# Performance work log

Hardware: AMD Instinct MI355X
Metric: run time of the kernel (lower is better)

The kernel has to match this reference:

```python
import jax, jax.numpy as jnp
import numpy as np

K = 4          # temporal_depth
IN_SIZE = 1024 # conv input channels
DN = ('NCDHW', 'OIDHW', 'NCDHW')


def setup_inputs() -> dict:
    key = jax.random.key(0)
    ks = jax.random.split(key, 12)
    B, T, C, H, W = 1, 8, IN_SIZE, 14, 14
    s = 0.02
    return {
        'videos': jax.random.normal(ks[0], (B, T, C, H, W), dtype=jnp.float32),
        # Conv3d(in_size, in_size, 3, padding='same')
        'conv1_w': jax.random.normal(ks[1], (IN_SIZE, IN_SIZE, 3, 3, 3), dtype=jnp.float32) * s,
        'conv1_b': jax.random.normal(ks[2], (IN_SIZE,), dtype=jnp.float32) * s,
        # Conv3d(in_size, 512, 3, padding='same')
        'conv2_w': jax.random.normal(ks[3], (512, IN_SIZE, 3, 3, 3), dtype=jnp.float32) * s,
        'conv2_b': jax.random.normal(ks[4], (512,), dtype=jnp.float32) * s,
        # Linear(512,512) -> Linear(512,512) -> Linear(512,128), torch (out,in) layout
        'l1_w': jax.random.normal(ks[5], (512, 512), dtype=jnp.float32) * s,
        'l1_b': jax.random.normal(ks[6], (512,), dtype=jnp.float32) * s,
        'l2_w': jax.random.normal(ks[7], (512, 512), dtype=jnp.float32) * s,
        'l2_b': jax.random.normal(ks[8], (512,), dtype=jnp.float32) * s,
        'l3_w': jax.random.normal(ks[9], (128, 512), dtype=jnp.float32) * s,
        'l3_b': jax.random.normal(ks[10], (128,), dtype=jnp.float32) * s,
    }


def reference(videos, conv1_w, conv1_b, conv2_w, conv2_b,
              l1_w, l1_b, l2_w, l2_b, l3_w, l3_b):
    B, T, C, H, W = videos.shape
    # prepend k zero frames, as in the torch code
    padded = jnp.concatenate(
        [jnp.zeros((B, K, C, H, W), videos.dtype), videos], axis=1)
    # window o covers padded frames [o, o+K) -> strictly-past original frames
    idx = jnp.arange(T)[:, None] + jnp.arange(K)[None, :]      # (T, K)
    win = padded[:, idx]                                        # (B, T, K, C, H, W)
    # permute(1,0,2,3): channels first, depth=K -> batch all windows together
    win = win.transpose(0, 1, 3, 2, 4, 5).reshape(B * T, C, K, H, W)
    # Conv3d + ReLU + Conv3d + ReLU, each with 'same' zero padding per window
    h = jax.lax.conv_general_dilated(win, conv1_w, (1, 1, 1), 'SAME',
                                     dimension_numbers=DN)
    h = jax.nn.relu(h + conv1_b[None, :, None, None, None])
    h = jax.lax.conv_general_dilated(h, conv2_w, (1, 1, 1), 'SAME',
                                     dimension_numbers=DN)
    h = jax.nn.relu(h + conv2_b[None, :, None, None, None])
    # MaxPool3d over the full (D,H,W) extent == global max per channel
    pooled = jnp.max(h, axis=(2, 3, 4))                         # (B*T, 512)
    x = jax.nn.relu(pooled @ l1_w.T + l1_b)
    x = jax.nn.relu(x @ l2_w.T + l2_b)
    x = jax.nn.relu(x @ l3_w.T + l3_b)                          # (B*T, 128)
    return x.reshape(B, T, 128)
```

## Files before the change

### kernel.cpp

```cpp
#include <hip/hip_runtime.h>

typedef __attribute__((ext_vector_type(8))) short short8;
typedef __attribute__((ext_vector_type(4))) float floatx4;
typedef __attribute__((ext_vector_type(4))) unsigned short ushort4v;

#define DEV __device__ __forceinline__

constexpr int M_TOT = 6272;
constexpr int M_PAD = 6400;

DEV void async_ld16(const void* g, void* l) {
  __builtin_amdgcn_global_load_lds(
      (const __attribute__((address_space(1))) unsigned int*)g,
      (__attribute__((address_space(3))) unsigned int*)l,
      16, 0, 0);
}

DEV unsigned short f2bf(float x) {
  union { float f; unsigned int u; } v; v.f = x;
  unsigned int u = v.u;
  u += 0x7FFFu + ((u >> 16) & 1u);
  return (unsigned short)(u >> 16);
}

DEV float bf2f(unsigned short s) {
  union { unsigned int u; float f; } v; v.u = ((unsigned int)s) << 16;
  return v.f;
}

__global__ void wtrans(const float* __restrict__ w, unsigned short* __restrict__ wt,
                       int total ) {
  __shared__ unsigned short l[256 * 27];
  const int tid  = threadIdx.x;
  const int base = blockIdx.x * 256;
  #pragma unroll 1
  for (int j = tid; j < 256 * 27; j += 256)
    l[j] = f2bf(w[(size_t)base * 27 + j]);
  __syncthreads();
  #pragma unroll 1
  for (int tap = 0; tap < 27; ++tap)
    wt[(size_t)tap * total + base + tid] = l[tid * 27 + tap];
}

__global__ void build_P1(const float* __restrict__ videos, unsigned short* __restrict__ P1) {
  const int f  = blockIdx.x;
  const int c0 = blockIdx.y * 64;
  const int tid = threadIdx.x;
  __shared__ unsigned short tile[64][196];

  #pragma unroll 1
  for (int it = 0; it < 49; ++it) {
    int idx = it * 256 + tid;
    int c = idx / 196, r = idx - c * 196;
    tile[c][r] = f2bf(videos[(size_t)(f * 1024 + c0 + c) * 196 + r]);
  }
  __syncthreads();

  const int c   = tid & 63;
  const int hwq = tid >> 6;
  #pragma unroll 1
  for (int s = 1; s <= 4; ++s) {
    int t = f + 5 - s;
    if (t > 7) continue;
    unsigned short* dst = P1 + (size_t)(t * 6 + s) * 256 * 1024 + (size_t)c0;
    #pragma unroll 1
    for (int it = 0; it < 49; ++it) {
      int hw = it * 4 + hwq;
      int h = hw / 14, w = hw - h * 14;
      dst[(size_t)((h + 1) * 16 + (w + 1)) * 1024 + c] = tile[c][hw];
    }
  }
}

template <int COUT, bool TCOND>
__global__ __launch_bounds__(512, 2) void conv_gemm(
    const unsigned short* __restrict__ P,
    const unsigned short* __restrict__ Wt,
    const unsigned int* __restrict__ sched,
    unsigned short* __restrict__ part)
{
  constexpr int CIN = 1024;
  __shared__ short lA[4][8192];
  __shared__ short lB[4][8192];
  const int tid  = threadIdx.x;
  const int wave = tid >> 6;
  const int lane = tid & 63;

  const unsigned int e = sched[blockIdx.x];
  const int x2   = e & 31;
  const int nidx = (e >> 5) & 3;
  const int zs   = (e >> 7) & 7;
  const int tap0 = (e >> 10) & 31;
  const int tap1 = (e >> 15) & 31;
  const int m0 = x2 * 256;
  const int n0 = nidx * 256;
  unsigned short* partOut = part + (size_t)zs * M_PAD * COUT;

  bool kdv[3] = {false, false, false};
  {
    const int cA = m0 / 196;
    int cB = (m0 + 255) / 196; if (cB > 31) cB = 31;
    for (int c = cA; c <= cB; ++c) {
      int t = c >> 2, d = c & 3;
      #pragma unroll
      for (int kd = 0; kd < 3; ++kd) {
        int s = d + kd;
        bool ok = (s >= 1) && (s <= 4);
        if (TCOND) ok = ok && (s >= 5 - t);
        kdv[kd] = kdv[kd] || ok;
      }
    }
  }

  const int arow = tid >> 2;
  const int aswz = (((tid & 3) ^ ((arow >> 1) & 3)) << 4);
  int aG[2], bG[2];
  #pragma unroll
  for (int q = 0; q < 2; ++q) {
    int m = m0 + q * 128 + arow;
    int t = m / 784;  int r2 = m - t * 784;
    int d = r2 / 196; int r3 = r2 - d * 196;
    int h = r3 / 14;  int w = r3 - h * 14;
    aG[q] = ((((t * 6 + d) * 16 + h) * 16 + w) * CIN) * 2 + aswz;
    bG[q] = (n0 + q * 128 + arow) * (CIN * 2) + aswz;
  }

  int nvt = 0;
  for (int tp = tap0; tp < tap1; ++tp) if (kdv[tp / 9]) ++nvt;
  const int steps = nvt * 32;
  int tap_s = tap0;
  while (tap_s < tap1 && !kdv[tap_s / 9]) ++tap_s;
  int c_s = 0;
  int stA = 0, stB = 0;
  auto setBases = [&]() {
    const int kd = tap_s / 9, rm = tap_s - kd * 9;
    const int kh = rm / 3, kw = rm - kh * 3;
    stA = ((((kd * 16) + kh) * 16 + kw) * CIN) * 2 + c_s * 2;
    stB = tap_s * (COUT * CIN * 2) + c_s * 2;
  };
  auto adv = [&]() {
    c_s += 32;
    if (c_s == CIN) { c_s = 0; do { ++tap_s; } while (tap_s < tap1 && !kdv[tap_s / 9]); }
  };

  const char* Pb = (const char*)P;
  const char* Wb = (const char*)Wt;
  char* lAc = (char*)&lA[0][0];
  char* lBc = (char*)&lB[0][0];

  const int nst = steps < 3 ? steps : 3;
  #pragma unroll 1
  for (int s = 0; s < nst; ++s) {
    setBases();
    char* dA = lAc + s * 16384;
    char* dB = lBc + s * 16384;
    async_ld16(Pb + aG[0] + stA, dA + tid * 16);
    async_ld16(Wb + bG[0] + stB, dB + tid * 16);
    async_ld16(Pb + aG[1] + stA, dA + 8192 + tid * 16);
    async_ld16(Wb + bG[1] + stB, dB + 8192 + tid * 16);
    adv();
  }
  if (nst >= 3)      asm volatile("s_waitcnt vmcnt(8)" ::: "memory");
  else if (nst == 2) asm volatile("s_waitcnt vmcnt(4)" ::: "memory");
  else               asm volatile("s_waitcnt vmcnt(0)" ::: "memory");
  __builtin_amdgcn_s_barrier();
  __builtin_amdgcn_sched_barrier(0);

  const int wm   = (wave >> 2) * 128;
  const int wn   = (wave & 3) * 64;
  const int quad = lane >> 4;
  const int l15  = lane & 15;
  const int segc = ((quad ^ ((l15 >> 1) & 3)) << 4);

  floatx4 acc[8][4];
  const floatx4 zero4 = {0.f, 0.f, 0.f, 0.f};
  #pragma unroll
  for (int i = 0; i < 8; ++i)
    #pragma unroll
    for (int j = 0; j < 4; ++j) acc[i][j] = zero4;

  #pragma unroll 1
  for (int t = 0; t < steps; ++t) {
    const char* Ap = lAc + (t & 3) * 16384;
    const char* Bp = lBc + (t & 3) * 16384;
    const bool h3s = (t + 3 < steps);
    const bool h2s = (t + 2 < steps);
    char* dA = lAc + ((t + 3) & 3) * 16384;
    char* dB = lBc + ((t + 3) & 3) * 16384;
    if (h3s) setBases();

    short8 b[4], a0[4];
    #pragma unroll
    for (int j = 0; j < 4; ++j)
      b[j] = *(const short8*)(Bp + ((wn + j * 16 + l15) << 6) + segc);
    #pragma unroll
    for (int i = 0; i < 4; ++i)
      a0[i] = *(const short8*)(Ap + ((wm + i * 16 + l15) << 6) + segc);
    if (h3s) {
      async_ld16(Pb + aG[0] + stA, dA + tid * 16);
      async_ld16(Wb + bG[0] + stB, dB + tid * 16);
    }
    asm volatile("s_waitcnt lgkmcnt(0)" ::: "memory");
    __builtin_amdgcn_sched_barrier(0);
    __builtin_amdgcn_s_setprio(1);
    #pragma unroll
    for (int i = 0; i < 4; ++i)
      #pragma unroll
      for (int j = 0; j < 4; ++j)
        acc[i][j] = __builtin_amdgcn_mfma_f32_16x16x32_bf16(a0[i], b[j], acc[i][j], 0, 0, 0);
    __builtin_amdgcn_s_setprio(0);

    short8 a1[4];
    #pragma unroll
    for (int i = 0; i < 4; ++i)
      a1[i] = *(const short8*)(Ap + ((wm + 64 + i * 16 + l15) << 6) + segc);
    if (h3s) {
      async_ld16(Pb + aG[1] + stA, dA + 8192 + tid * 16);
      async_ld16(Wb + bG[1] + stB, dB + 8192 + tid * 16);
      adv();
    }
    asm volatile("s_waitcnt lgkmcnt(0)" ::: "memory");
    __builtin_amdgcn_sched_barrier(0);
    __builtin_amdgcn_s_setprio(1);
    #pragma unroll
    for (int i = 0; i < 4; ++i)
      #pragma unroll
      for (int j = 0; j < 4; ++j)
        acc[4 + i][j] = __builtin_amdgcn_mfma_f32_16x16x32_bf16(a1[i], b[j], acc[4 + i][j], 0, 0, 0);
    __builtin_amdgcn_s_setprio(0);

    if (h3s)                asm volatile("s_waitcnt vmcnt(8)" ::: "memory");
    else if (h2s)           asm volatile("s_waitcnt vmcnt(4)" ::: "memory");
    else if (t + 1 < steps) asm volatile("s_waitcnt vmcnt(0)" ::: "memory");
    __builtin_amdgcn_sched_barrier(0);
    __builtin_amdgcn_s_barrier();
    __builtin_amdgcn_sched_barrier(0);
  }

  asm volatile("s_waitcnt vmcnt(0) lgkmcnt(0)" ::: "memory");
  __builtin_amdgcn_s_barrier();

  #pragma unroll
  for (int j = 0; j < 4; ++j) {
    const int o = n0 + wn + j * 16 + l15;
    #pragma unroll
    for (int i = 0; i < 8; ++i) {
      #pragma unroll
      for (int r = 0; r < 4; ++r) {
        int m = m0 + wm + i * 16 + quad * 4 + r;
        partOut[(size_t)m * COUT + o] = f2bf(acc[i][j][r]);
      }
    }
  }
}

__global__ void reduce_conv1(const unsigned short* __restrict__ part,
                             const float* __restrict__ bias,
                             unsigned short* __restrict__ P2) {
  const int idx = blockIdx.x * 256 + threadIdx.x;
  const int m  = idx >> 8;
  const int o4 = (idx & 255) * 4;
  const size_t ss = (size_t)M_PAD * 1024;
  const size_t base = (size_t)m * 1024 + o4;
  ushort4v p0 = *(const ushort4v*)(part + base);
  ushort4v p1 = *(const ushort4v*)(part + ss + base);
  ushort4v p2 = *(const ushort4v*)(part + 2 * ss + base);
  ushort4v out;
  #pragma unroll
  for (int k = 0; k < 4; ++k) {
    float v = bf2f(p0[k]) + bf2f(p1[k]) + bf2f(p2[k]) + bias[o4 + k];
    out[k] = f2bf(v > 0.f ? v : 0.f);
  }
  int t = m / 784;  int r2 = m - t * 784;
  int d = r2 / 196; int r3 = r2 - d * 196;
  int h = r3 / 14;  int w = r3 - h * 14;
  size_t didx = (size_t)(((t * 6 + d + 1) * 16 + (h + 1)) * 16 + (w + 1)) * 1024 + o4;
  *(ushort4v*)(P2 + didx) = out;
}

__global__ void reduce_conv2(const unsigned short* __restrict__ part,
                             const float* __restrict__ bias,
                             unsigned short* __restrict__ h2) {
  const int idx = blockIdx.x * 256 + threadIdx.x;
  const int m  = idx >> 7;
  const int o4 = (idx & 127) * 4;
  const size_t base = (size_t)m * 512 + o4;
  const size_t ss = (size_t)M_PAD * 512;
  float acc[4];
  #pragma unroll
  for (int k = 0; k < 4; ++k) acc[k] = bias[o4 + k];
  #pragma unroll
  for (int s = 0; s < 5; ++s) {
    ushort4v p = *(const ushort4v*)(part + (size_t)s * ss + base);
    #pragma unroll
    for (int k = 0; k < 4; ++k) acc[k] += bf2f(p[k]);
  }
  ushort4v out;
  #pragma unroll
  for (int k = 0; k < 4; ++k) out[k] = f2bf(acc[k] > 0.f ? acc[k] : 0.f);
  *(ushort4v*)(h2 + base) = out;
}

__global__ void pool1(const unsigned short* __restrict__ h2,
                      unsigned short* __restrict__ partial) {
  const int t = blockIdx.x / 28, ch = blockIdx.x % 28, o = threadIdx.x;
  const unsigned short* src = h2 + ((size_t)t * 784 + ch * 28) * 512 + o;
  unsigned short m = 0;
  #pragma unroll 4
  for (int i = 0; i < 28; ++i) { unsigned short v = src[(size_t)i * 512]; m = v > m ? v : m; }
  partial[((size_t)t * 28 + ch) * 512 + o] = m;
}

__global__ void pool2(const unsigned short* __restrict__ partial, float* __restrict__ pooled) {
  const int t = blockIdx.x, o = threadIdx.x;
  const unsigned short* src = partial + (size_t)t * 28 * 512 + o;
  unsigned short m = 0;
  #pragma unroll 4
  for (int i = 0; i < 28; ++i) { unsigned short v = src[(size_t)i * 512]; m = v > m ? v : m; }
  pooled[t * 512 + o] = bf2f(m);
}

__global__ void mlp_kernel(const float* __restrict__ pooled,
                           const float* __restrict__ w1, const float* __restrict__ b1,
                           const float* __restrict__ w2, const float* __restrict__ b2,
                           const float* __restrict__ w3, const float* __restrict__ b3,
                           float* __restrict__ out) {
  const int t = blockIdx.x, j = threadIdx.x;
  __shared__ float xa[512], xb[512];
  xa[j] = pooled[t * 512 + j];
  __syncthreads();
  {
    const float4* wr = (const float4*)(w1 + (size_t)j * 512);
    float s = b1[j];
    #pragma unroll 4
    for (int k = 0; k < 128; ++k) {
      float4 wv = wr[k];
      s += wv.x * xa[4*k] + wv.y * xa[4*k+1] + wv.z * xa[4*k+2] + wv.w * xa[4*k+3];
    }
    xb[j] = fmaxf(s, 0.f);
  }
  __syncthreads();
  {
    const float4* wr = (const float4*)(w2 + (size_t)j * 512);
    float s = b2[j];
    #pragma unroll 4
    for (int k = 0; k < 128; ++k) {
      float4 wv = wr[k];
      s += wv.x * xb[4*k] + wv.y * xb[4*k+1] + wv.z * xb[4*k+2] + wv.w * xb[4*k+3];
    }
    xa[j] = fmaxf(s, 0.f);
  }
  __syncthreads();
  if (j < 128) {
    const float4* wr = (const float4*)(w3 + (size_t)j * 512);
    float s = b3[j];
    #pragma unroll 4
    for (int k = 0; k < 128; ++k) {
      float4 wv = wr[k];
      s += wv.x * xa[4*k] + wv.y * xa[4*k+1] + wv.z * xa[4*k+2] + wv.w * xa[4*k+3];
    }
    out[t * 128 + j] = fmaxf(s, 0.f);
  }
}

static int build_sched(bool conv1, unsigned int* out) {
  const int nt = conv1 ? 4 : 2;
  unsigned int L[256];
  int cnt = 0;
  for (int n = 0; n < nt; ++n) {
    for (int x2 = 0; x2 < 25; ++x2) {
      const int m0 = x2 * 256;
      bool kdv[3] = {false, false, false};
      const int cA = m0 / 196;
      int cB = (m0 + 255) / 196; if (cB > 31) cB = 31;
      for (int c = cA; c <= cB; ++c) {
        int t = c >> 2, d = c & 3;
        for (int kd = 0; kd < 3; ++kd) {
          int s = d + kd;
          bool ok = (s >= 1 && s <= 4);
          if (conv1) ok = ok && (s >= 5 - t);
          kdv[kd] = kdv[kd] || ok;
        }
      }
      int vt[27], nv = 0;
      for (int tp = 0; tp < 27; ++tp) if (kdv[tp / 9]) vt[nv++] = tp;
      if (!nv) continue;
      const int ns = conv1 ? (nv / 9) : ((nv == 27) ? 5 : 4);
      for (int s = 0; s < ns; ++s) {
        int b0 = nv * s / ns, b1 = nv * (s + 1) / ns;
        int tp0 = vt[b0], tp1 = vt[b1 - 1] + 1;
        L[cnt++] = (unsigned int)(x2 | (n << 5) | (s << 7) | (tp0 << 10) | (tp1 << 15));
      }
    }
  }
  const int q = cnt / 8, r = cnt % 8;
  int pos = 0;
  for (int b = 0; b < 8; ++b) {
    const int nb = q + (b < r ? 1 : 0);
    for (int j = 0; j < nb; ++j) out[j * 8 + b] = L[pos++];
  }
  return cnt;
}

extern "C" void kernel_launch(void* const* d_in, const int* in_sizes, int n_in,
                              void* d_out, int out_size, void* d_ws, size_t ws_size,
                              hipStream_t stream) {
  const float* videos = (const float*)d_in[0];
  const float* c1w = (const float*)d_in[1];
  const float* c1b = (const float*)d_in[2];
  const float* c2w = (const float*)d_in[3];
  const float* c2b = (const float*)d_in[4];
  const float* l1w = (const float*)d_in[5];
  const float* l1b = (const float*)d_in[6];
  const float* l2w = (const float*)d_in[7];
  const float* l2b = (const float*)d_in[8];
  const float* l3w = (const float*)d_in[9];
  const float* l3b = (const float*)d_in[10];

  char* ws = (char*)d_ws;
  unsigned short* P12   = (unsigned short*)(ws);
  unsigned short* W1t   = (unsigned short*)(ws + 26738688);
  unsigned short* W2t   = (unsigned short*)(ws + 26738688);
  unsigned short* h2    = (unsigned short*)(ws + 55050240);
  float*          pooled= (float*)(ws + 61472768);
  unsigned short* ppart = (unsigned short*)(ws + 61489152);
  unsigned short* part  = (unsigned short*)(ws + 83361792);
  unsigned int* dsched1 = (unsigned int*)(ws + 122683392);
  unsigned int* dsched2 = (unsigned int*)(ws + 122684416);
  float* out = (float*)d_out;

  static unsigned int s1h[256], s2h[256];
  const int n1 = build_sched(true,  s1h);
  const int n2 = build_sched(false, s2h);
  hipMemcpyAsync(dsched1, s1h, sizeof(s1h), hipMemcpyHostToDevice, stream);
  hipMemcpyAsync(dsched2, s2h, sizeof(s2h), hipMemcpyHostToDevice, stream);

  hipMemsetAsync(ws, 0, 26738688, stream);
  hipMemsetAsync(part, 0, 39321600, stream);

  wtrans<<<4096, 256, 0, stream>>>(c1w, W1t, 1024 * 1024);
  build_P1<<<dim3(8, 16), 256, 0, stream>>>(videos, P12);

  conv_gemm<1024, true ><<<n1, 512, 0, stream>>>(P12, W1t, dsched1, part);

  wtrans<<<2048, 256, 0, stream>>>(c2w, W2t, 512 * 1024);
  reduce_conv1<<<6272, 256, 0, stream>>>(part, c1b, P12);
  hipMemsetAsync((char*)part + 32505856, 0, 262144, stream);

  conv_gemm<512, false><<<n2, 512, 0, stream>>>(P12, W2t, dsched2, part);
  reduce_conv2<<<3136, 256, 0, stream>>>(part, c2b, h2);

  pool1<<<224, 512, 0, stream>>>(h2, ppart);
  pool2<<<8, 512, 0, stream>>>(ppart, pooled);
  mlp_kernel<<<8, 512, 0, stream>>>(pooled, l1w, l1b, l2w, l2b, l3w, l3b, out);
}
```

Before: 762.0 us.

## Software-pipeline LDS fragment reads across steps with fine-grained lgkmcnt waits

```diff
diff --git a/kernel.cpp b/kernel.cpp
--- a/kernel.cpp
+++ b/kernel.cpp
@@ -1,6 +1,7 @@
 #include <hip/hip_runtime.h>
 
 typedef __attribute__((ext_vector_type(8))) short short8;
+typedef __attribute__((ext_vector_type(4))) int int4v;
 typedef __attribute__((ext_vector_type(4))) float floatx4;
 typedef __attribute__((ext_vector_type(4))) unsigned short ushort4v;
 
@@ -71,6 +72,13 @@
     }
   }
 }
+
+#define DSR(dst, addr, off) \
+  asm volatile("ds_read_b128 %0, %1 offset:" #off : "=&v"(dst) : "v"(addr))
+#define WAITL(n) \
+  asm volatile("s_waitcnt lgkmcnt(" #n ")" ::: "memory"); \
+  __builtin_amdgcn_sched_barrier(0)
+#define SB0 __builtin_amdgcn_sched_barrier(0)
 
 template <int COUT, bool TCOND>
 __global__ __launch_bounds__(512, 2) void conv_gemm(
@@ -147,10 +155,13 @@
   const char* Wb = (const char*)Wt;
   char* lAc = (char*)&lA[0][0];
   char* lBc = (char*)&lB[0][0];
-
-  const int nst = steps < 3 ? steps : 3;
+  const unsigned ldsA0 =
+      (unsigned)(size_t)(__attribute__((address_space(3))) char*)lAc;
+  const unsigned ldsB0 =
+      (unsigned)(size_t)(__attribute__((address_space(3))) char*)lBc;
+
   #pragma unroll 1
-  for (int s = 0; s < nst; ++s) {
+  for (int s = 0; s < 3; ++s) {
     setBases();
     char* dA = lAc + s * 16384;
     char* dB = lBc + s * 16384;
@@ -160,17 +171,17 @@
     async_ld16(Wb + bG[1] + stB, dB + 8192 + tid * 16);
     adv();
   }
-  if (nst >= 3)      asm volatile("s_waitcnt vmcnt(8)" ::: "memory");
-  else if (nst == 2) asm volatile("s_waitcnt vmcnt(4)" ::: "memory");
-  else               asm volatile("s_waitcnt vmcnt(0)" ::: "memory");
+  asm volatile("s_waitcnt vmcnt(4)" ::: "memory");
   __builtin_amdgcn_s_barrier();
-  __builtin_amdgcn_sched_barrier(0);
+  SB0;
 
   const int wm   = (wave >> 2) * 128;
   const int wn   = (wave & 3) * 64;
   const int quad = lane >> 4;
   const int l15  = lane & 15;
   const int segc = ((quad ^ ((l15 >> 1) & 3)) << 4);
+  const unsigned rowA = ((unsigned)(wm + l15) << 6) + segc;
+  const unsigned rowB = ((unsigned)(wn + l15) << 6) + segc;
 
   floatx4 acc[8][4];
   const floatx4 zero4 = {0.f, 0.f, 0.f, 0.f};
@@ -179,62 +190,95 @@
     #pragma unroll
     for (int j = 0; j < 4; ++j) acc[i][j] = zero4;
 
+  int4v pbE0, pbE1, pbE2, pbE3, paE0, paE1;
+  int4v pbO0, pbO1, pbO2, pbO3, paO0, paO1;
+
+  {
+    const unsigned aB = ldsA0 + rowA;
+    const unsigned bB = ldsB0 + rowB;
+    DSR(pbE0, bB, 0);
+    DSR(pbE1, bB, 1024);
+    DSR(pbE2, bB, 2048);
+    DSR(pbE3, bB, 3072);
+    DSR(paE0, aB, 0);
+    DSR(paE1, aB, 1024);
+  }
+  SB0;
+
+#define MFMA_GRP(ACCI, AV)                                                  \
+  {                                                                         \
+    short8 a_ = __builtin_bit_cast(short8, AV);                             \
+    acc[ACCI][0] = __builtin_amdgcn_mfma_f32_16x16x32_bf16(a_, bs0, acc[ACCI][0], 0, 0, 0); \
+    acc[ACCI][1] = __builtin_amdgcn_mfma_f32_16x16x32_bf16(a_, bs1, acc[ACCI][1], 0, 0, 0); \
+    acc[ACCI][2] = __builtin_amdgcn_mfma_f32_16x16x32_bf16(a_, bs2, acc[ACCI][2], 0, 0, 0); \
+    acc[ACCI][3] = __builtin_amdgcn_mfma_f32_16x16x32_bf16(a_, bs3, acc[ACCI][3], 0, 0, 0); \
+  }
+
+#define STEP_BODY(U, PB0, PB1, PB2, PB3, PA0, PA1, NB0, NB1, NB2, NB3, NA0, NA1) \
+  {                                                                         \
+    const int u_ = (U);                                                     \
+    const bool h3s = (u_ + 3 < steps);                                      \
+    const unsigned aB = ldsA0 + (unsigned)(u_ & 3) * 16384u + rowA;         \
+    int4v f2, f3, f4, f5, f6, f7;                                           \
+    DSR(f2, aB, 2048);                                                      \
+    DSR(f3, aB, 3072);                                                      \
+    DSR(f4, aB, 4096);                                                      \
+    DSR(f5, aB, 5120);                                                      \
+    DSR(f6, aB, 6144);                                                      \
+    DSR(f7, aB, 7168);                                                      \
+    SB0;                                                                    \
+    if (h3s) {                                                              \
+      setBases();                                                           \
+      char* dA = lAc + ((u_ + 3) & 3) * 16384;                              \
+      char* dB = lBc + ((u_ + 3) & 3) * 16384;                              \
+      async_ld16(Pb + aG[0] + stA, dA + tid * 16);                          \
+      async_ld16(Wb + bG[0] + stB, dB + tid * 16);                          \
+      async_ld16(Pb + aG[1] + stA, dA + 8192 + tid * 16);                   \
+      async_ld16(Wb + bG[1] + stB, dB + 8192 + tid * 16);                   \
+      adv();                                                                \
+    }                                                                       \
+    SB0;                                                                    \
+    __builtin_amdgcn_s_setprio(1);                                          \
+    short8 bs0, bs1, bs2, bs3;                                              \
+    WAITL(7);                                                               \
+    bs0 = __builtin_bit_cast(short8, PB0);                                  \
+    bs1 = __builtin_bit_cast(short8, PB1);                                  \
+    bs2 = __builtin_bit_cast(short8, PB2);                                  \
+    bs3 = __builtin_bit_cast(short8, PB3);                                  \
+    MFMA_GRP(0, PA0);                                                       \
+    WAITL(6); MFMA_GRP(1, PA1);                                             \
+    WAITL(5); MFMA_GRP(2, f2);                                              \
+    WAITL(4); MFMA_GRP(3, f3);                                              \
+    WAITL(3); MFMA_GRP(4, f4);                                              \
+    WAITL(2); MFMA_GRP(5, f5);                                              \
+    WAITL(1); MFMA_GRP(6, f6);                                              \
+    WAITL(0); MFMA_GRP(7, f7);                                              \
+    __builtin_amdgcn_s_setprio(0);                                          \
+    SB0;                                                                    \
+    if (u_ + 1 < steps) {                                                   \
+      const unsigned nA = ldsA0 + (unsigned)((u_ + 1) & 3) * 16384u + rowA; \
+      const unsigned nB = ldsB0 + (unsigned)((u_ + 1) & 3) * 16384u + rowB; \
+      DSR(NB0, nB, 0);                                                      \
+      DSR(NB1, nB, 1024);                                                   \
+      DSR(NB2, nB, 2048);                                                   \
+      DSR(NB3, nB, 3072);                                                   \
+      DSR(NA0, nA, 0);                                                      \
+      DSR(NA1, nA, 1024);                                                   \
+    }                                                                       \
+    SB0;                                                                    \
+    if (h3s) { asm volatile("s_waitcnt vmcnt(4)" ::: "memory"); }           \
+    else     { asm volatile("s_waitcnt vmcnt(0)" ::: "memory"); }           \
+    SB0;                                                                    \
+    __builtin_amdgcn_s_barrier();                                           \
+    SB0;                                                                    \
+  }
+
   #pragma unroll 1
-  for (int t = 0; t < steps; ++t) {
-    const char* Ap = lAc + (t & 3) * 16384;
-    const char* Bp = lBc + (t & 3) * 16384;
-    const bool h3s = (t + 3 < steps);
-    const bool h2s = (t + 2 < steps);
-    char* dA = lAc + ((t + 3) & 3) * 16384;
-    char* dB = lBc + ((t + 3) & 3) * 16384;
-    if (h3s) setBases();
-
-    short8 b[4], a0[4];
-    #pragma unroll
-    for (int j = 0; j < 4; ++j)
-      b[j] = *(const short8*)(Bp + ((wn + j * 16 + l15) << 6) + segc);
-    #pragma unroll
-    for (int i = 0; i < 4; ++i)
-      a0[i] = *(const short8*)(Ap + ((wm + i * 16 + l15) << 6) + segc);
-    if (h3s) {
-      async_ld16(Pb + aG[0] + stA, dA + tid * 16);
-      async_ld16(Wb + bG[0] + stB, dB + tid * 16);
-    }
-    asm volatile("s_waitcnt lgkmcnt(0)" ::: "memory");
-    __builtin_amdgcn_sched_barrier(0);
-    __builtin_amdgcn_s_setprio(1);
-    #pragma unroll
-    for (int i = 0; i < 4; ++i)
-      #pragma unroll
-      for (int j = 0; j < 4; ++j)
-        acc[i][j] = __builtin_amdgcn_mfma_f32_16x16x32_bf16(a0[i], b[j], acc[i][j], 0, 0, 0);
-    __builtin_amdgcn_s_setprio(0);
-
-    short8 a1[4];
-    #pragma unroll
-    for (int i = 0; i < 4; ++i)
-      a1[i] = *(const short8*)(Ap + ((wm + 64 + i * 16 + l15) << 6) + segc);
-    if (h3s) {
-      async_ld16(Pb + aG[1] + stA, dA + 8192 + tid * 16);
-      async_ld16(Wb + bG[1] + stB, dB + 8192 + tid * 16);
-      adv();
-    }
-    asm volatile("s_waitcnt lgkmcnt(0)" ::: "memory");
-    __builtin_amdgcn_sched_barrier(0);
-    __builtin_amdgcn_s_setprio(1);
-    #pragma unroll
-    for (int i = 0; i < 4; ++i)
-      #pragma unroll
-      for (int j = 0; j < 4; ++j)
-        acc[4 + i][j] = __builtin_amdgcn_mfma_f32_16x16x32_bf16(a1[i], b[j], acc[4 + i][j], 0, 0, 0);
-    __builtin_amdgcn_s_setprio(0);
-
-    if (h3s)                asm volatile("s_waitcnt vmcnt(8)" ::: "memory");
-    else if (h2s)           asm volatile("s_waitcnt vmcnt(4)" ::: "memory");
-    else if (t + 1 < steps) asm volatile("s_waitcnt vmcnt(0)" ::: "memory");
-    __builtin_amdgcn_sched_barrier(0);
-    __builtin_amdgcn_s_barrier();
-    __builtin_amdgcn_sched_barrier(0);
+  for (int t = 0; t < steps; t += 2) {
+    STEP_BODY(t,     pbE0, pbE1, pbE2, pbE3, paE0, paE1,
+                     pbO0, pbO1, pbO2, pbO3, paO0, paO1);
+    STEP_BODY(t + 1, pbO0, pbO1, pbO2, pbO3, paO0, paO1,
+                     pbE0, pbE1, pbE2, pbE3, paE0, paE1);
   }
 
   asm volatile("s_waitcnt vmcnt(0) lgkmcnt(0)" ::: "memory");
@@ -252,6 +296,8 @@
       }
     }
   }
+#undef STEP_BODY
+#undef MFMA_GRP
 }
 
 __global__ void reduce_conv1(const unsigned short* __restrict__ part,
```

After: 748.0 us. About the same (-1.8%).
